# Kernel optimization log

Measured on AMD Instinct MI355X. Metric: run time of the kernel, lower is better.

The kernel has to match this reference:

```python
import jax, jax.numpy as jnp
import numpy as np

BATCH = 16384
MAX_ACTIVE = 32
FEAT = 768
HIDDEN = 1024


def setup_inputs() -> dict:
    key = jax.random.key(0)
    k1, k2, k3, k4, k5, k6 = jax.random.split(key, 6)
    stm = jax.random.randint(k1, (BATCH, MAX_ACTIVE), 0, FEAT, dtype=jnp.int32)
    nstm = jax.random.randint(k2, (BATCH, MAX_ACTIVE), 0, FEAT, dtype=jnp.int32)
    # Linear params (PyTorch layout: weight is (out_features, in_features))
    ft_w = jax.random.normal(k3, (HIDDEN, FEAT), dtype=jnp.float32) * 0.05
    ft_b = jax.random.normal(k4, (HIDDEN,), dtype=jnp.float32) * 0.05
    out_w = jax.random.normal(k5, (1, 2 * HIDDEN), dtype=jnp.float32) * 0.05
    out_b = jax.random.normal(k6, (1,), dtype=jnp.float32) * 0.05
    return {"stm": stm, "nstm": nstm, "ft_w": ft_w, "ft_b": ft_b,
            "out_w": out_w, "out_b": out_b}


def sparse_to_dense(indices: jnp.ndarray, size: int = FEAT) -> jnp.ndarray:
    """(B, max_active) int indices with -1 padding -> (B, size) 0/1 float32."""
    b = indices.shape[0]
    valid = (indices >= 0).astype(jnp.float32)          # (B, A)
    cols = jnp.clip(indices, 0, size - 1)               # padded -> col 0, masked by `valid`
    rows = jnp.arange(b, dtype=jnp.int32)[:, None]      # (B, 1) broadcast
    dense = jnp.zeros((b, size), dtype=jnp.float32)
    # .max matches torch's set-to-1 semantics even if duplicate indices occur
    return dense.at[rows, cols].max(valid)


def reference(stm, nstm, ft_w, ft_b, out_w, out_b):
    stm_d = sparse_to_dense(stm)                        # (B, 768)
    nstm_d = sparse_to_dense(nstm)                      # (B, 768)
    stm_h = stm_d @ ft_w.T + ft_b                       # (B, H)
    nstm_h = nstm_d @ ft_w.T + ft_b                     # (B, H)
    hidden = jnp.concatenate([stm_h, nstm_h], axis=1)   # (B, 2H)
    hidden = jnp.clip(hidden, 0.0, 1.0)
    return jax.nn.sigmoid(hidden @ out_w.T + out_b)     # (B, 1)
```

## Files before the change

### kernel.cpp

```cpp
#include <hip/hip_runtime.h>
#include <stdint.h>

#define BATCH 16384
#define MAXA 32
#define FEAT 768
#define HIDDEN 1024

__global__ __launch_bounds__(256) void prep_quant(const float* __restrict__ ftw,
                                                  uint8_t* __restrict__ wQ,
                                                  float* __restrict__ scale) {
  const int h0 = blockIdx.x * 8;
  const int hloc = threadIdx.x >> 5;
  const int l32 = threadIdx.x & 31;
  const int h = h0 + hloc;

  float w[24];
  float amax = 0.f;
  const float* __restrict__ src = ftw + (size_t)h * FEAT;
#pragma unroll
  for (int k = 0; k < 24; ++k) {
    w[k] = src[l32 + 32 * k];
    amax = fmaxf(amax, fabsf(w[k]));
  }
#pragma unroll
  for (int m = 1; m <= 16; m <<= 1)
    amax = fmaxf(amax, __shfl_xor(amax, m, 64));
  amax = fmaxf(amax, 1e-20f);
  if (l32 == 0) scale[h] = amax / 127.f;
  const float inv = 127.f / amax;

  __shared__ __align__(16) uint8_t tile[FEAT * 8];
#pragma unroll
  for (int k = 0; k < 24; ++k) {
    int q = __float2int_rn(w[k] * inv);
    tile[(l32 + 32 * k) * 8 + hloc] = (uint8_t)(q + 128);
  }
  __syncthreads();

#pragma unroll
  for (int p = 0; p < 3; ++p) {
    int f = threadIdx.x + 256 * p;
    unsigned long long v = *(const unsigned long long*)&tile[f * 8];
    *(unsigned long long*)(wQ + (size_t)f * HIDDEN + h0) = v;
  }

  if (blockIdx.x == 0)
    ((uint32_t*)(wQ + (size_t)FEAT * HIDDEN))[threadIdx.x] = 0x80808080u;
}

__device__ __forceinline__ void acc16(uint32_t* acc, uint4 w) {
  acc[0] += __builtin_amdgcn_perm(0u, w.x, 0x0c010c00u);
  acc[1] += __builtin_amdgcn_perm(0u, w.x, 0x0c030c02u);
  acc[2] += __builtin_amdgcn_perm(0u, w.y, 0x0c010c00u);
  acc[3] += __builtin_amdgcn_perm(0u, w.y, 0x0c030c02u);
  acc[4] += __builtin_amdgcn_perm(0u, w.z, 0x0c010c00u);
  acc[5] += __builtin_amdgcn_perm(0u, w.z, 0x0c030c02u);
  acc[6] += __builtin_amdgcn_perm(0u, w.w, 0x0c010c00u);
  acc[7] += __builtin_amdgcn_perm(0u, w.w, 0x0c030c02u);
}

__global__ __launch_bounds__(256) void nn_fwd(
    const int* __restrict__ stm, const int* __restrict__ nstm,
    const uint8_t* __restrict__ wQ, const float* __restrict__ scale,
    const float* __restrict__ bias, const float* __restrict__ outw,
    const float* __restrict__ outb, float* __restrict__ out)
{
  const int lane = threadIdx.x & 63;
  const int wid  = threadIdx.x >> 6;
  const int rsel = wid >> 1;
  const int side = wid & 1;
  const int row  = blockIdx.x * 2 + rsel;
  const int pos  = lane & 31;

  const int* __restrict__ src = side ? nstm : stm;
  int idx = src[row * MAXA + pos];
  bool valid = idx >= 0;
#pragma unroll
  for (int j = 0; j < 31; ++j) {
    int other = __shfl(idx, j, 64);
    if (j < pos && other == idx) valid = false;
  }
  const int fmap = valid ? idx : FEAT;

  uint32_t acc[8];
#pragma unroll
  for (int k = 0; k < 8; ++k) acc[k] = 0u;

#pragma unroll
  for (int j = 0; j < 32; ++j) {
    int f_ = __builtin_amdgcn_readlane(fmap, j);
    uint4 w_ = ((const uint4*)(wQ + (size_t)f_ * HIDDEN))[lane];
    acc16(acc, w_);
  }

  const int DB = 32 * 128;

  const int hbase = lane * 16;
  const float4* s4 = (const float4*)(scale + hbase);
  const float4* b4 = (const float4*)(bias + hbase);
  const float4* o4 = (const float4*)(outw + side * HIDDEN + hbase);
  float partial = 0.f;
#pragma unroll
  for (int q = 0; q < 4; ++q) {
    float4 s = s4[q], b = b4[q], o = o4[q];
    uint32_t a0 = acc[2 * q], a1 = acc[2 * q + 1];
    int q0 = (int)(a0 & 0xffffu) - DB;
    int q1 = (int)(a0 >> 16)    - DB;
    int q2 = (int)(a1 & 0xffffu) - DB;
    int q3 = (int)(a1 >> 16)    - DB;
    float h0 = fminf(fmaxf(fmaf((float)q0, s.x, b.x), 0.f), 1.f);
    float h1 = fminf(fmaxf(fmaf((float)q1, s.y, b.y), 0.f), 1.f);
    float h2 = fminf(fmaxf(fmaf((float)q2, s.z, b.z), 0.f), 1.f);
    float h3 = fminf(fmaxf(fmaf((float)q3, s.w, b.w), 0.f), 1.f);
    partial += h0 * o.x + h1 * o.y + h2 * o.z + h3 * o.w;
  }
#pragma unroll
  for (int off = 32; off > 0; off >>= 1)
    partial += __shfl_down(partial, off, 64);

  __shared__ float lpart[2];
  if (side == 1 && lane == 0) lpart[rsel] = partial;
  __syncthreads();
  if (side == 0 && lane == 0) {
    float y = partial + lpart[rsel] + outb[0];
    out[row] = 1.f / (1.f + __expf(-y));
  }
}

extern "C" void kernel_launch(void* const* d_in, const int* in_sizes, int n_in,
                              void* d_out, int out_size, void* d_ws, size_t ws_size,
                              hipStream_t stream) {
  const int*   stm  = (const int*)d_in[0];
  const int*   nstm = (const int*)d_in[1];
  const float* ftw  = (const float*)d_in[2];
  const float* ftb  = (const float*)d_in[3];
  const float* outw = (const float*)d_in[4];
  const float* outb = (const float*)d_in[5];

  uint8_t* wQ    = (uint8_t*)d_ws;
  float*   scale = (float*)(wQ + (size_t)(FEAT + 1) * HIDDEN);

  prep_quant<<<HIDDEN / 8, 256, 0, stream>>>(ftw, wQ, scale);
  nn_fwd<<<BATCH / 2, 256, 0, stream>>>(stm, nstm, wQ, scale, ftb, outw, outb,
                                        (float*)d_out);
}
```

Measured before the change: 123.9 us.

## Replace sparse gather-accumulate with dense int8 MFMA over one-hot feature tiles

Each block now builds one-hot int8 activation rows for 64 batch rows in LDS and multiplies them against the quantized weight matrix with 32x32x32 int8 MFMA instructions. The weights are pre-packed into an MFMA-friendly tiled layout and streamed through a double-buffered LDS tile. The per-lane scattered row gathers and byte-unpack adds are replaced by dense matrix math. It trades sparse work for dense compute and uses large LDS at one block per CU. The output reduction moves to atomics plus a separate sigmoid kernel, adding a launch.

After: 140.8 us. 13.7% more time.

```diff
diff --git a/kernel.cpp b/kernel.cpp
--- a/kernel.cpp
+++ b/kernel.cpp
@@ -6,9 +6,19 @@
 #define FEAT 768
 #define HIDDEN 1024
 
+#define KC 24
+#define NT 32
+#define ASTRIDE 784
+#define AWBYTES (32 * ASTRIDE)
+#define BTILE (KC * 1024)
+
+typedef int v4i  __attribute__((ext_vector_type(4)));
+typedef int v16i __attribute__((ext_vector_type(16)));
+
 __global__ __launch_bounds__(256) void prep_quant(const float* __restrict__ ftw,
-                                                  uint8_t* __restrict__ wQ,
-                                                  float* __restrict__ scale) {
+                                                  uint8_t* __restrict__ Bf,
+                                                  float* __restrict__ scale,
+                                                  float* __restrict__ outz) {
   const int h0 = blockIdx.x * 8;
   const int hloc = threadIdx.x >> 5;
   const int l32 = threadIdx.x & 31;
@@ -29,102 +39,146 @@
   if (l32 == 0) scale[h] = amax / 127.f;
   const float inv = 127.f / amax;
 
-  __shared__ __align__(16) uint8_t tile[FEAT * 8];
+  __shared__ __align__(16) uint8_t tile[8][ASTRIDE];
 #pragma unroll
   for (int k = 0; k < 24; ++k) {
     int q = __float2int_rn(w[k] * inv);
-    tile[(l32 + 32 * k) * 8 + hloc] = (uint8_t)(q + 128);
+    tile[hloc][l32 + 32 * k] = (uint8_t)(int8_t)q;
   }
   __syncthreads();
 
-#pragma unroll
-  for (int p = 0; p < 3; ++p) {
-    int f = threadIdx.x + 256 * p;
-    unsigned long long v = *(const unsigned long long*)&tile[f * 8];
-    *(unsigned long long*)(wQ + (size_t)f * HIDDEN + h0) = v;
-  }
-
-  if (blockIdx.x == 0)
-    ((uint32_t*)(wQ + (size_t)FEAT * HIDDEN))[threadIdx.x] = 0x80808080u;
-}
-
-__device__ __forceinline__ void acc16(uint32_t* acc, uint4 w) {
-  acc[0] += __builtin_amdgcn_perm(0u, w.x, 0x0c010c00u);
-  acc[1] += __builtin_amdgcn_perm(0u, w.x, 0x0c030c02u);
-  acc[2] += __builtin_amdgcn_perm(0u, w.y, 0x0c010c00u);
-  acc[3] += __builtin_amdgcn_perm(0u, w.y, 0x0c030c02u);
-  acc[4] += __builtin_amdgcn_perm(0u, w.z, 0x0c010c00u);
-  acc[5] += __builtin_amdgcn_perm(0u, w.z, 0x0c030c02u);
-  acc[6] += __builtin_amdgcn_perm(0u, w.w, 0x0c010c00u);
-  acc[7] += __builtin_amdgcn_perm(0u, w.w, 0x0c030c02u);
-}
-
-__global__ __launch_bounds__(256) void nn_fwd(
+  for (int g = threadIdx.x; g < 8 * 48; g += 256) {
+    int hl = g / 48, fg = g % 48;
+    int kc = fg >> 1, lh = fg & 1;
+    int hh = h0 + hl;
+    uint4 v = *(const uint4*)&tile[hl][fg * 16];
+    size_t daddr = ((size_t)((hh >> 5) * KC + kc) << 10) +
+                   (size_t)(((lh << 5) | (hh & 31)) << 4);
+    *(uint4*)(Bf + daddr) = v;
+  }
+
+  if (threadIdx.x < 128)
+    outz[blockIdx.x * 128 + threadIdx.x] = 0.f;
+}
+
+__global__ __launch_bounds__(256, 1) void nn_mfma(
     const int* __restrict__ stm, const int* __restrict__ nstm,
-    const uint8_t* __restrict__ wQ, const float* __restrict__ scale,
+    const uint8_t* __restrict__ Bf, const float* __restrict__ scale,
     const float* __restrict__ bias, const float* __restrict__ outw,
-    const float* __restrict__ outb, float* __restrict__ out)
+    float* __restrict__ outz)
 {
-  const int lane = threadIdx.x & 63;
-  const int wid  = threadIdx.x >> 6;
-  const int rsel = wid >> 1;
+  const int tid  = threadIdx.x;
+  const int lane = tid & 63;
+  const int wid  = tid >> 6;
   const int side = wid & 1;
-  const int row  = blockIdx.x * 2 + rsel;
-  const int pos  = lane & 31;
-
-  const int* __restrict__ src = side ? nstm : stm;
-  int idx = src[row * MAXA + pos];
-  bool valid = idx >= 0;
-#pragma unroll
-  for (int j = 0; j < 31; ++j) {
-    int other = __shfl(idx, j, 64);
-    if (j < pos && other == idx) valid = false;
-  }
-  const int fmap = valid ? idx : FEAT;
-
-  uint32_t acc[8];
-#pragma unroll
-  for (int k = 0; k < 8; ++k) acc[k] = 0u;
-
-#pragma unroll
-  for (int j = 0; j < 32; ++j) {
-    int f_ = __builtin_amdgcn_readlane(fmap, j);
-    uint4 w_ = ((const uint4*)(wQ + (size_t)f_ * HIDDEN))[lane];
-    acc16(acc, w_);
-  }
-
-  const int DB = 32 * 128;
-
-  const int hbase = lane * 16;
-  const float4* s4 = (const float4*)(scale + hbase);
-  const float4* b4 = (const float4*)(bias + hbase);
-  const float4* o4 = (const float4*)(outw + side * HIDDEN + hbase);
-  float partial = 0.f;
-#pragma unroll
-  for (int q = 0; q < 4; ++q) {
-    float4 s = s4[q], b = b4[q], o = o4[q];
-    uint32_t a0 = acc[2 * q], a1 = acc[2 * q + 1];
-    int q0 = (int)(a0 & 0xffffu) - DB;
-    int q1 = (int)(a0 >> 16)    - DB;
-    int q2 = (int)(a1 & 0xffffu) - DB;
-    int q3 = (int)(a1 >> 16)    - DB;
-    float h0 = fminf(fmaxf(fmaf((float)q0, s.x, b.x), 0.f), 1.f);
-    float h1 = fminf(fmaxf(fmaf((float)q1, s.y, b.y), 0.f), 1.f);
-    float h2 = fminf(fmaxf(fmaf((float)q2, s.z, b.z), 0.f), 1.f);
-    float h3 = fminf(fmaxf(fmaf((float)q3, s.w, b.w), 0.f), 1.f);
-    partial += h0 * o.x + h1 * o.y + h2 * o.z + h3 * o.w;
-  }
-#pragma unroll
-  for (int off = 32; off > 0; off >>= 1)
-    partial += __shfl_down(partial, off, 64);
-
-  __shared__ float lpart[2];
-  if (side == 1 && lane == 0) lpart[rsel] = partial;
+  const int rgrp = wid >> 1;
+  const int r0   = blockIdx.x * 64 + rgrp * 32;
+  const int l31  = lane & 31;
+  const int lh   = lane >> 5;
+
+  __shared__ __align__(16) uint8_t Ash[4 * AWBYTES];
+  __shared__ __align__(16) uint8_t Bbuf[2][BTILE];
+
+  uint8_t* Aw = Ash + wid * AWBYTES;
+
+  uint4 st[6];
+  {
+    const uint4* g = (const uint4*)Bf;
+#pragma unroll
+    for (int s = 0; s < 6; ++s) st[s] = g[s * 256 + tid];
+  }
+
+  const uint4 z4 = {0u, 0u, 0u, 0u};
+#pragma unroll
+  for (int it = 0; it < 25; ++it) {
+    int off = it * 1024 + lane * 16;
+    if (off < AWBYTES) *(uint4*)(Aw + off) = z4;
+  }
+  const int* __restrict__ isrc = side ? nstm : stm;
+#pragma unroll
+  for (int i = 0; i < 16; ++i) {
+    int row = i * 2 + lh;
+    int idx = isrc[(r0 + row) * MAXA + l31];
+    if (idx >= 0) Aw[row * ASTRIDE + idx] = 1;
+  }
+  v4i areg[KC];
+#pragma unroll
+  for (int kc = 0; kc < KC; ++kc)
+    areg[kc] = *(const v4i*)(Aw + l31 * ASTRIDE + kc * 32 + lh * 16);
+
+#pragma unroll
+  for (int s = 0; s < 6; ++s) ((uint4*)Bbuf[0])[s * 256 + tid] = st[s];
   __syncthreads();
-  if (side == 0 && lane == 0) {
-    float y = partial + lpart[rsel] + outb[0];
-    out[row] = 1.f / (1.f + __expf(-y));
-  }
+
+  float* sbo = (float*)Ash;
+  {
+    const float4* gs = (const float4*)scale;
+    const float4* gb = (const float4*)bias;
+    const float4* go = (const float4*)outw;
+    float4* d = (float4*)sbo;
+    d[tid]       = gs[tid];
+    d[256 + tid] = gb[tid];
+    d[512 + tid] = go[tid];
+    d[768 + tid] = go[256 + tid];
+  }
+  __syncthreads();
+
+  float prow[16];
+#pragma unroll
+  for (int r = 0; r < 16; ++r) prow[r] = 0.f;
+
+#pragma unroll 1
+  for (int nt = 0; nt < NT; ++nt) {
+    const int p = nt & 1;
+    if (nt + 1 < NT) {
+      const uint4* g = (const uint4*)(Bf + (size_t)(nt + 1) * BTILE);
+#pragma unroll
+      for (int s = 0; s < 6; ++s) st[s] = g[s * 256 + tid];
+    }
+    v16i acc;
+#pragma unroll
+    for (int r = 0; r < 16; ++r) acc[r] = 0;
+    const uint8_t* bp = Bbuf[p];
+#pragma unroll
+    for (int kc = 0; kc < KC; ++kc) {
+      v4i b = *(const v4i*)(bp + kc * 1024 + lane * 16);
+      acc = __builtin_amdgcn_mfma_i32_32x32x32_i8(areg[kc], b, acc, 0, 0, 0);
+    }
+    float s  = sbo[nt * 32 + l31];
+    float bb = sbo[1024 + nt * 32 + l31];
+    float o  = sbo[2048 + side * HIDDEN + nt * 32 + l31];
+#pragma unroll
+    for (int r = 0; r < 16; ++r) {
+      float hv = fminf(fmaxf(fmaf((float)acc[r], s, bb), 0.f), 1.f);
+      prow[r] = fmaf(hv, o, prow[r]);
+    }
+    if (nt + 1 < NT) {
+      uint4* d = (uint4*)Bbuf[p ^ 1];
+#pragma unroll
+      for (int s2 = 0; s2 < 6; ++s2) d[s2 * 256 + tid] = st[s2];
+    }
+    __syncthreads();
+  }
+
+#pragma unroll
+  for (int off = 16; off >= 1; off >>= 1)
+#pragma unroll
+    for (int r = 0; r < 16; ++r) prow[r] += __shfl_xor(prow[r], off, 64);
+
+  if (l31 == 0) {
+#pragma unroll
+    for (int r = 0; r < 16; ++r) {
+      int row = (r & 3) + 8 * (r >> 2) + 4 * lh;
+      atomicAdd(&outz[r0 + row], prow[r]);
+    }
+  }
+}
+
+__global__ __launch_bounds__(256) void nn_finish(float* __restrict__ outz,
+                                                 const float* __restrict__ outb) {
+  const int i = blockIdx.x * 256 + threadIdx.x;
+  float y = outz[i] + outb[0];
+  outz[i] = 1.f / (1.f + __expf(-y));
 }
 
 extern "C" void kernel_launch(void* const* d_in, const int* in_sizes, int n_in,
@@ -137,10 +191,11 @@
   const float* outw = (const float*)d_in[4];
   const float* outb = (const float*)d_in[5];
 
-  uint8_t* wQ    = (uint8_t*)d_ws;
-  float*   scale = (float*)(wQ + (size_t)(FEAT + 1) * HIDDEN);
-
-  prep_quant<<<HIDDEN / 8, 256, 0, stream>>>(ftw, wQ, scale);
-  nn_fwd<<<BATCH / 2, 256, 0, stream>>>(stm, nstm, wQ, scale, ftb, outw, outb,
-                                        (float*)d_out);
-}
+  uint8_t* Bf    = (uint8_t*)d_ws;
+  float*   scale = (float*)(Bf + (size_t)FEAT * HIDDEN);
+  float*   outz  = (float*)d_out;
+
+  prep_quant<<<HIDDEN / 8, 256, 0, stream>>>(ftw, Bf, scale, outz);
+  nn_mfma<<<BATCH / 64, 256, 0, stream>>>(stm, nstm, Bf, scale, ftb, outw, outz);
+  nn_finish<<<BATCH / 256, 256, 0, stream>>>(outz, outb);
+}
```
